# Performance work log

Measured on AMD Instinct MI355X. Metric: run time of the kernel, lower is better.

## Reference

```python
import jax, jax.numpy as jnp
import numpy as np

NUM_USERS = 100000
NUM_ITEMS = 50000
NUM_EDGES = 2000000
DIM = 64
NUM_REL = 5


def setup_inputs() -> dict:
    key = jax.random.key(0)
    k1, k2, k3, k4, k5, k6 = jax.random.split(key, 6)
    u_features = jax.random.normal(k1, (NUM_USERS, DIM), dtype=jnp.float32)
    i_features = jax.random.normal(k2, (NUM_ITEMS, DIM), dtype=jnp.float32)
    edge_user = jax.random.randint(k3, (NUM_EDGES,), 0, NUM_USERS, dtype=jnp.int64)
    edge_item = jax.random.randint(k4, (NUM_EDGES,), 0, NUM_ITEMS, dtype=jnp.int64)
    # per-relation Linear params, torch convention: y = x @ W[r].T + b[r]
    W = jax.random.normal(k5, (NUM_REL, DIM, DIM), dtype=jnp.float32) * (1.0 / np.sqrt(DIM))
    b = jax.random.normal(k6, (NUM_REL, DIM), dtype=jnp.float32) * 0.01
    return {"u_features": u_features, "i_features": i_features,
            "edge_user": edge_user, "edge_item": edge_item, "W": W, "b": b}


def reference(u_features, i_features, edge_user, edge_item, W, b):
    # gather edge endpoint features: [E, D]
    edge_u = u_features[edge_user]
    edge_i = i_features[edge_item]
    num_rel = W.shape[0]
    # per relation: sum((edge_u @ W[r].T + b[r]) * edge_i, axis=1) -> [E]
    # loop over small fixed relation count to avoid [E, R, D] intermediate
    cols = [jnp.sum((edge_u @ W[r].T + b[r]) * edge_i, axis=1)
            for r in range(num_rel)]
    return jnp.stack(cols, axis=1)  # [E, R]
```

## Files before the change

### kernel.cpp

```cpp
#include <hip/hip_runtime.h>
#include <stdint.h>

#define NREL 5
#define D 64
#define Q_BYTES 320
#define NT 21

typedef __attribute__((ext_vector_type(8))) short short8;
typedef __attribute__((ext_vector_type(4))) float f32x4;

static __device__ __forceinline__ short f2bf(float f) {
    uint32_t u = __float_as_uint(f);
    u += 0x7FFFu + ((u >> 16) & 1u);
    return (short)(u >> 16);
}

#if defined(__has_builtin)
#if __has_builtin(__builtin_amdgcn_sdot4)
#define HAVE_SDOT4 1
#endif
#endif
#ifdef HAVE_SDOT4
static __device__ __forceinline__ int SDOT4(uint32_t a, uint32_t b, int c) {
    return __builtin_amdgcn_sdot4((int)a, (int)b, c, false);
}
#else
static __device__ __forceinline__ int SDOT4(uint32_t a, uint32_t b, int c) {
    c += ((int)(a << 24) >> 24) * ((int)(b << 24) >> 24);
    c += ((int)(a << 16) >> 24) * ((int)(b << 16) >> 24);
    c += ((int)(a << 8) >> 24) * ((int)(b << 8) >> 24);
    c += ((int)a >> 24) * ((int)b >> 24);
    return c;
}
#endif

__global__ __launch_bounds__(256) void w_prep_kernel(
    const float* __restrict__ W, const float* __restrict__ b, short* __restrict__ Wf)
{
    const int tid = blockIdx.x * 256 + threadIdx.x;
    if (tid >= NT * 2 * 64) return;
    const int lane = tid & 63;
    const int h = (tid >> 6) & 1;
    const int nt = tid >> 7;
    const int ln = lane & 15, quad = lane >> 4;
    const int n = nt * 16 + ln;
    uint32_t w[4];
#pragma unroll
    for (int p = 0; p < 4; ++p) {
        uint32_t lo, hi;
#pragma unroll
        for (int s = 0; s < 2; ++s) {
            const int j = p * 2 + s;
            const int d = h * 32 + quad * 8 + j;
            float v;
            if (nt < 20) v = W[(n >> 6) * (D * D) + d * D + (n & 63)];
            else         v = (ln < NREL) ? b[ln * D + d] : 0.f;
            if (s == 0) lo = (uint16_t)f2bf(v); else hi = (uint16_t)f2bf(v);
        }
        w[p] = lo | (hi << 16);
    }
    *(uint4*)(Wf + (size_t)tid * 8) = make_uint4(w[0], w[1], w[2], w[3]);
}

__global__ __launch_bounds__(256) void u_quant_kernel(
    const float* __restrict__ uf,
    uint32_t* __restrict__ uq,
    float* __restrict__ uscale,
    int nRows)
{
    const int gid = blockIdx.x * 256 + threadIdx.x;
    const int row = gid >> 4;
    const int t = gid & 15;
    if (row >= nRows) return;
    const float* rp = uf + (size_t)row * D;
    const float v0 = rp[t], v1 = rp[16 + t], v2 = rp[32 + t], v3 = rp[48 + t];
    float m = fmaxf(fmaxf(fabsf(v0), fabsf(v1)), fmaxf(fabsf(v2), fabsf(v3)));
    m = fmaxf(m, __shfl_xor(m, 1));
    m = fmaxf(m, __shfl_xor(m, 2));
    m = fmaxf(m, __shfl_xor(m, 4));
    m = fmaxf(m, __shfl_xor(m, 8));
    m = fmaxf(m, 1e-20f);
    const float qs = 127.0f / m;
    const int q0 = (int)rintf(v0 * qs);
    const int q1 = (int)rintf(v1 * qs);
    const int q2 = (int)rintf(v2 * qs);
    const int q3 = (int)rintf(v3 * qs);
    uq[(size_t)row * 16 + t] = ((uint32_t)(uint8_t)(int8_t)q0)
                             | ((uint32_t)(uint8_t)(int8_t)q1 << 8)
                             | ((uint32_t)(uint8_t)(int8_t)q2 << 16)
                             | ((uint32_t)(uint8_t)(int8_t)q3 << 24);
    if (t == 0) uscale[row] = m * (1.0f / 127.0f);
}

__global__ __launch_bounds__(256) void item_transform_kernel(
    const float* __restrict__ i_feat,
    const short* __restrict__ Wf,
    char* __restrict__ qrecs,
    float* __restrict__ sc,
    int nItems)
{
    const int lane = threadIdx.x & 63;
    const int wv = threadIdx.x >> 6;
    const int m0 = blockIdx.x * 64 + wv * 16;
    const int ln = lane & 15, quad = lane >> 4;

    int rowA = m0 + ln;
    if (rowA >= nItems) rowA = nItems - 1;
    const float* ap = i_feat + (size_t)rowA * D + quad * 8;
    short8 af[2];
#pragma unroll
    for (int h = 0; h < 2; ++h) {
        const float4 x = *(const float4*)(ap + h * 32);
        const float4 y = *(const float4*)(ap + h * 32 + 4);
        short8 a;
        a[0] = f2bf(x.x); a[1] = f2bf(x.y); a[2] = f2bf(x.z); a[3] = f2bf(x.w);
        a[4] = f2bf(y.x); a[5] = f2bf(y.y); a[6] = f2bf(y.z); a[7] = f2bf(y.w);
        af[h] = a;
    }

    f32x4 acc[NT];
#pragma unroll
    for (int nt = 0; nt < NT; ++nt) acc[nt] = (f32x4){0.f, 0.f, 0.f, 0.f};

#pragma unroll
    for (int nt = 0; nt < NT; ++nt) {
        const short8 b0 = *(const short8*)(Wf + ((size_t)(nt * 2 + 0) * 64 + lane) * 8);
        acc[nt] = __builtin_amdgcn_mfma_f32_16x16x32_bf16(af[0], b0, acc[nt], 0, 0, 0);
        const short8 b1 = *(const short8*)(Wf + ((size_t)(nt * 2 + 1) * 64 + lane) * 8);
        acc[nt] = __builtin_amdgcn_mfma_f32_16x16x32_bf16(af[1], b1, acc[nt], 0, 0, 0);
    }

#pragma unroll
    for (int g = 0; g < 4; ++g) {
        const int item = m0 + quad * 4 + g;
        const bool ok = (item < nItems);
        char* rec = qrecs + (size_t)item * Q_BYTES;
#pragma unroll
        for (int r = 0; r < NREL; ++r) {
            const float v0 = acc[4 * r + 0][g];
            const float v1 = acc[4 * r + 1][g];
            const float v2 = acc[4 * r + 2][g];
            const float v3 = acc[4 * r + 3][g];
            float m = fmaxf(fmaxf(fabsf(v0), fabsf(v1)), fmaxf(fabsf(v2), fabsf(v3)));
            m = fmaxf(m, __shfl_xor(m, 1));
            m = fmaxf(m, __shfl_xor(m, 2));
            m = fmaxf(m, __shfl_xor(m, 4));
            m = fmaxf(m, __shfl_xor(m, 8));
            m = fmaxf(m, 1e-20f);
            const float qs = 127.0f / m;
            const uint32_t pw = ((uint32_t)(uint8_t)(int8_t)(int)rintf(v0 * qs))
                              | ((uint32_t)(uint8_t)(int8_t)(int)rintf(v1 * qs) << 8)
                              | ((uint32_t)(uint8_t)(int8_t)(int)rintf(v2 * qs) << 16)
                              | ((uint32_t)(uint8_t)(int8_t)(int)rintf(v3 * qs) << 24);
            if (ok) {
                *(uint32_t*)(rec + r * D + ln * 4) = pw;
                if (ln == 0) sc[(size_t)item * 16 + r] = m * (1.0f / 127.0f);
            }
        }
        if (ok && ln < NREL) sc[(size_t)item * 16 + NREL + ln] = acc[20][g];
    }
}

__global__ __launch_bounds__(256) void edge_kernel(
    const uint32_t* __restrict__ u_q,
    const float* __restrict__ u_scale,
    const int* __restrict__ edge_user,
    const int* __restrict__ edge_item,
    const char* __restrict__ qrecs,
    const float* __restrict__ sc,
    float* __restrict__ out,
    int nE)
{
    const int lane = threadIdx.x & 63;
    const int wave = (blockIdx.x * 256 + threadIdx.x) >> 6;
    const int es = lane >> 2;
    const int c = lane & 3;

    const long e = (long)wave * 16 + es;
    if (e >= nE) return;

    const int iu = edge_user[e];
    const int ii = edge_item[e];
    const uint4 uv = *(const uint4*)(u_q + (size_t)iu * 16 + c * 4);
    const char* rec = qrecs + (size_t)ii * Q_BYTES;

    int s[NREL];
#pragma unroll
    for (int r = 0; r < NREL; ++r) {
        const uint4 yv = *(const uint4*)(rec + r * D + c * 16);
        int t = SDOT4(uv.x, yv.x, 0);
        t = SDOT4(uv.y, yv.y, t);
        t = SDOT4(uv.z, yv.z, t);
        s[r] = SDOT4(uv.w, yv.w, t);
    }
#pragma unroll
    for (int r = 0; r < NREL; ++r) {
        s[r] += __shfl_xor(s[r], 1);
        s[r] += __shfl_xor(s[r], 2);
    }
    const float us = u_scale[iu];
    const float* scp = sc + (size_t)ii * 16;
    out[e * NREL + c] = fmaf((float)s[c], us * scp[c], scp[NREL + c]);
    if (c == 0)
        out[e * NREL + 4] = fmaf((float)s[4], us * scp[4], scp[NREL + 4]);
}

extern "C" void kernel_launch(void* const* d_in, const int* in_sizes, int n_in,
                              void* d_out, int out_size, void* d_ws, size_t ws_size,
                              hipStream_t stream) {
    const float* u_feat    = (const float*)d_in[0];
    const float* i_feat    = (const float*)d_in[1];
    const int*   edge_user = (const int*)d_in[2];
    const int*   edge_item = (const int*)d_in[3];
    const float* W         = (const float*)d_in[4];
    const float* b         = (const float*)d_in[5];
    float* out = (float*)d_out;

    const int nUsers = in_sizes[0] / D;
    const int nItems = in_sizes[1] / D;
    const int nE = in_sizes[2];

    char* qrecs = (char*)d_ws;
    size_t off = ((size_t)nItems * Q_BYTES + 255) & ~(size_t)255;
    float* sc = (float*)((char*)d_ws + off);
    off += ((size_t)nItems * 16 * sizeof(float) + 255) & ~(size_t)255;
    uint32_t* u_q = (uint32_t*)((char*)d_ws + off);
    off += ((size_t)nUsers * D + 255) & ~(size_t)255;
    float* u_scale = (float*)((char*)d_ws + off);
    off += ((size_t)nUsers * sizeof(float) + 255) & ~(size_t)255;
    short* Wf = (short*)((char*)d_ws + off);

    {
        const int threads = NT * 2 * 64;
        w_prep_kernel<<<(threads + 255) / 256, 256, 0, stream>>>(W, b, Wf);
    }
    {
        const int threads = nUsers * 16;
        u_quant_kernel<<<(threads + 255) / 256, 256, 0, stream>>>(u_feat, u_q, u_scale, nUsers);
    }
    {
        const int blocks = (nItems + 63) / 64;
        item_transform_kernel<<<blocks, 256, 0, stream>>>(i_feat, Wf, qrecs, sc, nItems);
    }
    {
        const long waves = ((long)nE + 15) / 16;
        const long blocks = (waves + 3) / 4;
        edge_kernel<<<(int)blocks, 256, 0, stream>>>(u_q, u_scale, edge_user, edge_item,
                                                     qrecs, sc, out, nE);
    }
}
```

Before: 284.1 us.

## Bucket edges by item range and map buckets to XCDs for L2 locality

Adds a three-kernel counting sort (histogram, scan, scatter) that groups edges into 8 buckets by item index. The edge kernel then assigns each bucket to blocks with blockIdx%8 equal to the bucket, so each XCD's L2 only sees one-eighth of the 16 MB quantized item records. Edges are packed into 64-bit keys and outputs are written by original edge index. The cost is extra passes over the edge arrays (reads plus a 16 MB scattered write), a single-block scan, and uncoalesced output writes.

```diff
diff --git a/kernel.cpp b/kernel.cpp
--- a/kernel.cpp
+++ b/kernel.cpp
@@ -5,6 +5,8 @@
 #define D 64
 #define Q_BYTES 320
 #define NT 21
+#define NB 8
+#define CHUNK 2048
 
 typedef __attribute__((ext_vector_type(8))) short short8;
 typedef __attribute__((ext_vector_type(4))) float f32x4;
@@ -47,7 +49,7 @@
     uint32_t w[4];
 #pragma unroll
     for (int p = 0; p < 4; ++p) {
-        uint32_t lo, hi;
+        uint32_t lo = 0, hi = 0;
 #pragma unroll
         for (int s = 0; s < 2; ++s) {
             const int j = p * 2 + s;
@@ -161,48 +163,145 @@
     }
 }
 
+__global__ __launch_bounds__(256) void hist_kernel(
+    const int* __restrict__ edge_item, int nE, int bucketDiv,
+    int* __restrict__ blkHist)
+{
+    __shared__ int cnt[NB];
+    if (threadIdx.x < NB) cnt[threadIdx.x] = 0;
+    __syncthreads();
+    const long start = (long)blockIdx.x * CHUNK;
+#pragma unroll
+    for (int k = 0; k < CHUNK / 256; ++k) {
+        const long e = start + k * 256 + threadIdx.x;
+        if (e < nE) atomicAdd(&cnt[edge_item[e] / bucketDiv], 1);
+    }
+    __syncthreads();
+    if (threadIdx.x < NB) blkHist[blockIdx.x * NB + threadIdx.x] = cnt[threadIdx.x];
+}
+
+__global__ __launch_bounds__(512) void scan_kernel(
+    int* __restrict__ blkHist, int nBlocks, int* __restrict__ bucketBase)
+{
+    __shared__ int tot[NB];
+    __shared__ int base[NB + 1];
+    const int lane = threadIdx.x & 63;
+    const int b = threadIdx.x >> 6;
+    int carry = 0;
+    for (int c0 = 0; c0 < nBlocks; c0 += 64) {
+        const int idx = c0 + lane;
+        int v = (idx < nBlocks) ? blkHist[idx * NB + b] : 0;
+        int s = v;
+#pragma unroll
+        for (int d = 1; d < 64; d <<= 1) {
+            int t = __shfl_up(s, d);
+            if (lane >= d) s += t;
+        }
+        if (idx < nBlocks) blkHist[idx * NB + b] = carry + s - v;
+        carry += __shfl(s, 63);
+    }
+    if (lane == 0) tot[b] = carry;
+    __syncthreads();
+    if (threadIdx.x == 0) {
+        int s = 0;
+#pragma unroll
+        for (int i = 0; i < NB; ++i) { base[i] = s; s += tot[i]; }
+        base[NB] = s;
+#pragma unroll
+        for (int i = 0; i <= NB; ++i) bucketBase[i] = base[i];
+    }
+    __syncthreads();
+    const int add = base[b];
+    for (int c0 = 0; c0 < nBlocks; c0 += 64) {
+        const int idx = c0 + lane;
+        if (idx < nBlocks) blkHist[idx * NB + b] += add;
+    }
+}
+
+__global__ __launch_bounds__(256) void scatter_kernel(
+    const int* __restrict__ edge_user, const int* __restrict__ edge_item,
+    int nE, int bucketDiv, const int* __restrict__ blkHist,
+    unsigned long long* __restrict__ sorted)
+{
+    __shared__ int cnt[NB];
+    __shared__ int base[NB];
+    if (threadIdx.x < NB) {
+        cnt[threadIdx.x] = 0;
+        base[threadIdx.x] = blkHist[blockIdx.x * NB + threadIdx.x];
+    }
+    __syncthreads();
+    const long start = (long)blockIdx.x * CHUNK;
+#pragma unroll
+    for (int k = 0; k < CHUNK / 256; ++k) {
+        const long e = start + k * 256 + threadIdx.x;
+        if (e < nE) {
+            const int iu = edge_user[e];
+            const int ii = edge_item[e];
+            const int b = ii / bucketDiv;
+            const int rank = atomicAdd(&cnt[b], 1);
+            const unsigned long long pk = (unsigned long long)(uint32_t)iu
+                                        | ((unsigned long long)(uint32_t)ii << 17)
+                                        | ((unsigned long long)e << 33);
+            sorted[base[b] + rank] = pk;
+        }
+    }
+}
+
 __global__ __launch_bounds__(256) void edge_kernel(
     const uint32_t* __restrict__ u_q,
     const float* __restrict__ u_scale,
-    const int* __restrict__ edge_user,
-    const int* __restrict__ edge_item,
+    const unsigned long long* __restrict__ sorted,
+    const int* __restrict__ bucketBase,
     const char* __restrict__ qrecs,
     const float* __restrict__ sc,
-    float* __restrict__ out,
-    int nE)
-{
+    float* __restrict__ out)
+{
+    const int b = blockIdx.x & 7;
+    const int seg = blockIdx.x >> 3;
+    const int nSeg = gridDim.x >> 3;
+    const int s0 = bucketBase[b], s1 = bucketBase[b + 1];
+    const int cnt = s1 - s0;
+    const int per = (cnt + nSeg - 1) / nSeg;
+    const int p0 = s0 + seg * per;
+    const int p1 = min(p0 + per, s1);
+
     const int lane = threadIdx.x & 63;
-    const int wave = (blockIdx.x * 256 + threadIdx.x) >> 6;
+    const int wv = threadIdx.x >> 6;
     const int es = lane >> 2;
     const int c = lane & 3;
 
-    const long e = (long)wave * 16 + es;
-    if (e >= nE) return;
-
-    const int iu = edge_user[e];
-    const int ii = edge_item[e];
-    const uint4 uv = *(const uint4*)(u_q + (size_t)iu * 16 + c * 4);
-    const char* rec = qrecs + (size_t)ii * Q_BYTES;
-
-    int s[NREL];
-#pragma unroll
-    for (int r = 0; r < NREL; ++r) {
-        const uint4 yv = *(const uint4*)(rec + r * D + c * 16);
-        int t = SDOT4(uv.x, yv.x, 0);
-        t = SDOT4(uv.y, yv.y, t);
-        t = SDOT4(uv.z, yv.z, t);
-        s[r] = SDOT4(uv.w, yv.w, t);
-    }
-#pragma unroll
-    for (int r = 0; r < NREL; ++r) {
-        s[r] += __shfl_xor(s[r], 1);
-        s[r] += __shfl_xor(s[r], 2);
-    }
-    const float us = u_scale[iu];
-    const float* scp = sc + (size_t)ii * 16;
-    out[e * NREL + c] = fmaf((float)s[c], us * scp[c], scp[NREL + c]);
-    if (c == 0)
-        out[e * NREL + 4] = fmaf((float)s[4], us * scp[4], scp[NREL + 4]);
+    for (int q0 = p0 + wv * 16; q0 < p1; q0 += 64) {
+        const int pos = q0 + es;
+        if (pos < p1) {
+            const unsigned long long pk = sorted[pos];
+            const int iu = (int)(pk & 0x1FFFF);
+            const int ii = (int)((pk >> 17) & 0xFFFF);
+            const long e = (long)(pk >> 33);
+
+            const uint4 uv = *(const uint4*)(u_q + (size_t)iu * 16 + c * 4);
+            const char* rec = qrecs + (size_t)ii * Q_BYTES;
+
+            int s[NREL];
+#pragma unroll
+            for (int r = 0; r < NREL; ++r) {
+                const uint4 yv = *(const uint4*)(rec + r * D + c * 16);
+                int t = SDOT4(uv.x, yv.x, 0);
+                t = SDOT4(uv.y, yv.y, t);
+                t = SDOT4(uv.z, yv.z, t);
+                s[r] = SDOT4(uv.w, yv.w, t);
+            }
+#pragma unroll
+            for (int r = 0; r < NREL; ++r) {
+                s[r] += __shfl_xor(s[r], 1);
+                s[r] += __shfl_xor(s[r], 2);
+            }
+            const float us = u_scale[iu];
+            const float* scp = sc + (size_t)ii * 16;
+            out[e * NREL + c] = fmaf((float)s[c], us * scp[c], scp[NREL + c]);
+            if (c == 0)
+                out[e * NREL + 4] = fmaf((float)s[4], us * scp[4], scp[NREL + 4]);
+        }
+    }
 }
 
 extern "C" void kernel_launch(void* const* d_in, const int* in_sizes, int n_in,
@@ -219,9 +318,12 @@
     const int nUsers = in_sizes[0] / D;
     const int nItems = in_sizes[1] / D;
     const int nE = in_sizes[2];
-
+    const int bucketDiv = (nItems + NB - 1) / NB;
+    const int nBlocksSort = (nE + CHUNK - 1) / CHUNK;
+
+    size_t off = 0;
     char* qrecs = (char*)d_ws;
-    size_t off = ((size_t)nItems * Q_BYTES + 255) & ~(size_t)255;
+    off += ((size_t)nItems * Q_BYTES + 255) & ~(size_t)255;
     float* sc = (float*)((char*)d_ws + off);
     off += ((size_t)nItems * 16 * sizeof(float) + 255) & ~(size_t)255;
     uint32_t* u_q = (uint32_t*)((char*)d_ws + off);
@@ -229,6 +331,12 @@
     float* u_scale = (float*)((char*)d_ws + off);
     off += ((size_t)nUsers * sizeof(float) + 255) & ~(size_t)255;
     short* Wf = (short*)((char*)d_ws + off);
+    off += ((size_t)NT * 2 * 64 * 8 * sizeof(short) + 255) & ~(size_t)255;
+    int* blkHist = (int*)((char*)d_ws + off);
+    off += ((size_t)nBlocksSort * NB * sizeof(int) + 255) & ~(size_t)255;
+    int* bucketBase = (int*)((char*)d_ws + off);
+    off += 256;
+    unsigned long long* sorted = (unsigned long long*)((char*)d_ws + off);
 
     {
         const int threads = NT * 2 * 64;
@@ -242,10 +350,10 @@
         const int blocks = (nItems + 63) / 64;
         item_transform_kernel<<<blocks, 256, 0, stream>>>(i_feat, Wf, qrecs, sc, nItems);
     }
-    {
-        const long waves = ((long)nE + 15) / 16;
-        const long blocks = (waves + 3) / 4;
-        edge_kernel<<<(int)blocks, 256, 0, stream>>>(u_q, u_scale, edge_user, edge_item,
-                                                     qrecs, sc, out, nE);
-    }
-}
+    hist_kernel<<<nBlocksSort, 256, 0, stream>>>(edge_item, nE, bucketDiv, blkHist);
+    scan_kernel<<<1, 512, 0, stream>>>(blkHist, nBlocksSort, bucketBase);
+    scatter_kernel<<<nBlocksSort, 256, 0, stream>>>(edge_user, edge_item, nE, bucketDiv,
+                                                    blkHist, sorted);
+    edge_kernel<<<1280, 256, 0, stream>>>(u_q, u_scale, sorted, bucketBase,
+                                          qrecs, sc, out);
+}
```

Measured after the change: 276.9 us. -2.6%, faster.
